# Performance work log

Hardware: AMD Instinct MI355X
Metric: run time of the kernel (lower is better)

## Reference

```python
import jax, jax.numpy as jnp
import numpy as np

N = 100000
E = 1600000
D = 64

def setup_inputs() -> dict:
    key = jax.random.key(0)
    k1, k2, k3, k4, k5, k6 = jax.random.split(key, 6)
    h = jax.random.normal(k1, (N, D), dtype=jnp.float32)
    w = jax.random.uniform(k2, (E, 1), dtype=jnp.float32)
    src = jax.random.randint(k3, (E,), 0, N, dtype=jnp.int32)
    dst = jax.random.randint(k4, (E,), 0, N, dtype=jnp.int32)
    W = jax.random.normal(k5, (D, 2 * D), dtype=jnp.float32) / np.sqrt(2 * D)
    b = jax.random.normal(k6, (D,), dtype=jnp.float32) * 0.01
    return {"h": h, "w": w, "src": src, "dst": dst, "W": W, "b": b}

def reference(h, w, src, dst, W, b):
    # messages: per-edge weight times gathered source features  [E, D]
    m = w * h[src]
    # scatter-sum into destination nodes  [N, D]
    agg = jax.ops.segment_sum(m, dst, num_segments=N)
    # concat self + aggregated, then linear: [N, 2D] @ [2D, D] + b
    return jnp.concatenate([h, agg], axis=1) @ W.T + b
```

## Files before the change

kernel.cpp:

```cpp
#include <hip/hip_runtime.h>

#define D 64
#define CAP 32
#define WQ_BITS 15
#define WQ_MAX 32767.0f
#define NSHARDS 8

typedef int   int4v   __attribute__((ext_vector_type(4)));
typedef float float4v __attribute__((ext_vector_type(4)));

__device__ __forceinline__ ushort f2bf(float x) {
    unsigned u = __float_as_uint(x);
    unsigned r = (u + 0x7fff + ((u >> 16) & 1)) >> 16;
    return (ushort)r;
}
__device__ __forceinline__ float bf2f(ushort u) {
    return __uint_as_float(((unsigned)u) << 16);
}

__global__ __launch_bounds__(256) void scatter_shard_kernel(
    const int* __restrict__ src, const int* __restrict__ dst,
    const float* __restrict__ w, int* __restrict__ cursor,
    unsigned* __restrict__ ovBits, unsigned* __restrict__ pairs,
    int E, int N)
{
    int shard   = blockIdx.x & (NSHARDS - 1);
    int slice   = blockIdx.x >> 3;
    int nSlices = gridDim.x >> 3;
    int n8 = (N + NSHARDS - 1) / NSHARDS;
    int lo = shard * n8;
    int hi = min(N, lo + n8);

    int e4 = E >> 2;
    for (int gi = slice * 256 + threadIdx.x; gi < e4; gi += nSlices * 256) {
        int e0 = gi * 4;
        int4v   d4 = __builtin_nontemporal_load((const int4v*)&dst[e0]);
        int4v   s4 = __builtin_nontemporal_load((const int4v*)&src[e0]);
        float4v w4 = __builtin_nontemporal_load((const float4v*)&w[e0]);
        #pragma unroll
        for (int i = 0; i < 4; ++i) {
            int d = d4[i];
            if (d >= lo && d < hi) {
                int e = e0 + i;
                int pos = atomicAdd(&cursor[d], 1);
                if (pos < CAP) {
                    float wv = fminf(fmaxf(w4[i], 0.f), 1.f);
                    unsigned wq = (unsigned)(wv * WQ_MAX + 0.5f);
                    pairs[(size_t)d * CAP + pos] =
                        ((unsigned)s4[i] << WQ_BITS) | wq;
                } else {
                    atomicOr(&ovBits[e >> 5], 1u << (e & 31));
                }
            }
        }
    }
    for (int e = e4 * 4 + slice * 256 + threadIdx.x; e < E; e += nSlices * 256) {
        int d = dst[e];
        if (d >= lo && d < hi) {
            int pos = atomicAdd(&cursor[d], 1);
            if (pos < CAP) {
                float wv = fminf(fmaxf(w[e], 0.f), 1.f);
                unsigned wq = (unsigned)(wv * WQ_MAX + 0.5f);
                pairs[(size_t)d * CAP + pos] =
                    ((unsigned)src[e] << WQ_BITS) | wq;
            } else {
                atomicOr(&ovBits[e >> 5], 1u << (e & 31));
            }
        }
    }
}

__global__ __launch_bounds__(256) void gemm_fused_kernel(
    const float* __restrict__ h, const float* __restrict__ W,
    const float* __restrict__ b, float* __restrict__ out,
    ushort* __restrict__ g, int N)
{
    __shared__ float Wt[128 * 64];
    __shared__ float Xt[64 * 64];
    int tid = threadIdx.x;

    for (int idx = tid; idx < 128 * 64; idx += 256) {
        int j = idx & 63;
        int k = idx >> 6;
        Wt[k * 64 + j] = W[j * 128 + k];
    }

    int n0blk = blockIdx.x * 64;
    {
        int n = tid & 63;
        int krow = tid >> 6;
        int nn = min(n0blk + n, N - 1);
        #pragma unroll
        for (int c = 0; c < 4; ++c) {
            int k0 = (krow + c * 4) * 4;
            float4 v = *(const float4*)&h[(size_t)nn * D + k0];
            Xt[(k0 + 0) * 64 + n] = v.x;
            Xt[(k0 + 1) * 64 + n] = v.y;
            Xt[(k0 + 2) * 64 + n] = v.z;
            Xt[(k0 + 3) * 64 + n] = v.w;
        }
    }
    __syncthreads();

    int j0 = (tid & 15) * 4;
    int nb = (tid >> 4) * 4;

    float4 bv = *(const float4*)&b[j0];
    float accS[4][4], accG[4][4];
    #pragma unroll
    for (int i = 0; i < 4; ++i) {
        accS[i][0] = bv.x; accS[i][1] = bv.y; accS[i][2] = bv.z; accS[i][3] = bv.w;
        accG[i][0] = 0.f;  accG[i][1] = 0.f;  accG[i][2] = 0.f;  accG[i][3] = 0.f;
    }

    #pragma unroll 4
    for (int k = 0; k < 64; ++k) {
        float4 xv = *(const float4*)&Xt[k * 64 + nb];
        float4 w1 = *(const float4*)&Wt[k * 64 + j0];
        float4 w2 = *(const float4*)&Wt[(k + 64) * 64 + j0];
        #pragma unroll
        for (int i = 0; i < 4; ++i) {
            float x = (&xv.x)[i];
            accS[i][0] += x * w1.x; accS[i][1] += x * w1.y;
            accS[i][2] += x * w1.z; accS[i][3] += x * w1.w;
            accG[i][0] += x * w2.x; accG[i][1] += x * w2.y;
            accG[i][2] += x * w2.z; accG[i][3] += x * w2.w;
        }
    }

    #pragma unroll
    for (int i = 0; i < 4; ++i) {
        int n = n0blk + nb + i;
        if (n < N) {
            *(float4*)&out[(size_t)n * D + j0] =
                make_float4(accS[i][0], accS[i][1], accS[i][2], accS[i][3]);
            ushort4 gv;
            gv.x = f2bf(accG[i][0]); gv.y = f2bf(accG[i][1]);
            gv.z = f2bf(accG[i][2]); gv.w = f2bf(accG[i][3]);
            *(ushort4*)&g[(size_t)n * D + j0] = gv;
        }
    }
}

__global__ __launch_bounds__(256) void final_agg_kernel(
    const ushort* __restrict__ g, const unsigned* __restrict__ pairs,
    const int* __restrict__ cursor, float* __restrict__ out, int N)
{
    int wave = threadIdx.x >> 6;
    int lane = threadIdx.x & 63;
    int n = blockIdx.x * 4 + wave;
    if (n >= N) return;
    int cnt = min(cursor[n], CAP);
    unsigned mycode = (lane < CAP) ? pairs[(size_t)n * CAP + lane] : 0u;
    float acc = out[(size_t)n * D + lane];

    const float wscale = 1.0f / WQ_MAX;
    int j = 0;
    for (; j + 16 <= cnt; j += 16) {
        unsigned c[16];
        float v[16];
        #pragma unroll
        for (int u = 0; u < 16; ++u) c[u] = __shfl(mycode, j + u);
        #pragma unroll
        for (int u = 0; u < 16; ++u)
            v[u] = bf2f(g[(size_t)(c[u] >> WQ_BITS) * D + lane]);
        #pragma unroll
        for (int u = 0; u < 16; ++u)
            acc += (float)(c[u] & 0x7fffu) * wscale * v[u];
    }
    for (; j + 8 <= cnt; j += 8) {
        unsigned c[8];
        float v[8];
        #pragma unroll
        for (int u = 0; u < 8; ++u) c[u] = __shfl(mycode, j + u);
        #pragma unroll
        for (int u = 0; u < 8; ++u)
            v[u] = bf2f(g[(size_t)(c[u] >> WQ_BITS) * D + lane]);
        #pragma unroll
        for (int u = 0; u < 8; ++u)
            acc += (float)(c[u] & 0x7fffu) * wscale * v[u];
    }
    for (; j + 4 <= cnt; j += 4) {
        unsigned c[4];
        float v[4];
        #pragma unroll
        for (int u = 0; u < 4; ++u) c[u] = __shfl(mycode, j + u);
        #pragma unroll
        for (int u = 0; u < 4; ++u)
            v[u] = bf2f(g[(size_t)(c[u] >> WQ_BITS) * D + lane]);
        #pragma unroll
        for (int u = 0; u < 4; ++u)
            acc += (float)(c[u] & 0x7fffu) * wscale * v[u];
    }
    for (; j < cnt; ++j) {
        unsigned c = __shfl(mycode, j);
        acc += (float)(c & 0x7fffu) * wscale *
               bf2f(g[(size_t)(c >> WQ_BITS) * D + lane]);
    }
    out[(size_t)n * D + lane] = acc;
}

__global__ __launch_bounds__(256) void overflow_kernel(
    const unsigned* __restrict__ ovBits, const int* __restrict__ src,
    const int* __restrict__ dst, const float* __restrict__ w,
    const ushort* __restrict__ g, float* __restrict__ out, int numWords)
{
    int idx = blockIdx.x * 256 + threadIdx.x;
    for (int wi = idx; wi < numWords; wi += gridDim.x * 256) {
        unsigned bits = ovBits[wi];
        while (bits) {
            int bit = __ffs(bits) - 1;
            bits &= bits - 1;
            int e = wi * 32 + bit;
            int s = src[e], d = dst[e];
            float wv = w[e];
            for (int f = 0; f < D; ++f)
                atomicAdd(&out[(size_t)d * D + f], wv * bf2f(g[(size_t)s * D + f]));
        }
    }
}

__global__ __launch_bounds__(256) void edge_scatter_kernel(
    const float* __restrict__ h, const float* __restrict__ w,
    const int* __restrict__ src, const int* __restrict__ dst,
    float* __restrict__ agg, int E)
{
    int e = blockIdx.x * 4 + (threadIdx.x >> 6);
    int lane = threadIdx.x & 63;
    if (e >= E) return;
    float val = w[e] * h[(size_t)src[e] * D + lane];
    atomicAdd(&agg[(size_t)dst[e] * D + lane], val);
}

__global__ __launch_bounds__(256) void out_linear_kernel(
    const float* __restrict__ h, const float* __restrict__ agg,
    const float* __restrict__ W, const float* __restrict__ b,
    float* __restrict__ out, int N)
{
    __shared__ float Wt[128 * 64];
    int lane = threadIdx.x & 63;
    int waveInBlock = threadIdx.x >> 6;
    int wavesPerBlock = blockDim.x >> 6;
    for (int idx = threadIdx.x; idx < 128 * 64; idx += blockDim.x) {
        int j = idx & 63;
        int k = idx >> 6;
        Wt[k * 64 + j] = W[j * 128 + k];
    }
    __syncthreads();
    float bj = b[lane];
    int wavesPerGrid = gridDim.x * wavesPerBlock;
    for (int n = blockIdx.x * wavesPerBlock + waveInBlock; n < N; n += wavesPerGrid) {
        float hreg = h[(size_t)n * D + lane];
        float areg = agg[(size_t)n * D + lane];
        float acc = bj;
        #pragma unroll
        for (int k = 0; k < 64; ++k) {
            float hk = __shfl(hreg, k, 64);
            float ak = __shfl(areg, k, 64);
            acc += hk * Wt[k * 64 + lane];
            acc += ak * Wt[(k + 64) * 64 + lane];
        }
        out[(size_t)n * D + lane] = acc;
    }
}

extern "C" void kernel_launch(void* const* d_in, const int* in_sizes, int n_in,
                              void* d_out, int out_size, void* d_ws, size_t ws_size,
                              hipStream_t stream) {
    const float* h   = (const float*)d_in[0];
    const float* w   = (const float*)d_in[1];
    const int*   src = (const int*)d_in[2];
    const int*   dst = (const int*)d_in[3];
    const float* W   = (const float*)d_in[4];
    const float* b   = (const float*)d_in[5];
    float* out = (float*)d_out;

    int N = in_sizes[0] / D;
    int E = in_sizes[1];
    int numWords = (E + 31) / 32;

    auto align256 = [](size_t x) { return (x + 255) & ~(size_t)255; };
    size_t cursorB = align256((size_t)N * 4);
    size_t ovB     = align256((size_t)numWords * 4);
    size_t pairsB  = align256((size_t)N * CAP * 4);
    size_t gB      = align256((size_t)N * D * 2);
    size_t need = cursorB + ovB + pairsB + gB;

    if (ws_size >= need && N <= (1 << 17)) {
        char* p = (char*)d_ws;
        int*      cursor = (int*)p;       p += cursorB;
        unsigned* ovBits = (unsigned*)p;  p += ovB;
        unsigned* pairs  = (unsigned*)p;  p += pairsB;
        ushort*   g      = (ushort*)p;

        hipMemsetAsync(cursor, 0, cursorB + ovB, stream);

        scatter_shard_kernel<<<4096, 256, 0, stream>>>(src, dst, w, cursor,
                                                       ovBits, pairs, E, N);
        gemm_fused_kernel<<<(N + 63) / 64, 256, 0, stream>>>(h, W, b, out, g, N);
        final_agg_kernel<<<(N + 3) / 4, 256, 0, stream>>>(g, pairs, cursor, out, N);
        overflow_kernel<<<64, 256, 0, stream>>>(ovBits, src, dst, w, g, out, numWords);
    } else {
        float* agg = out;
        hipMemsetAsync(agg, 0, (size_t)N * D * 4, stream);
        edge_scatter_kernel<<<(E + 3) / 4, 256, 0, stream>>>(h, w, src, dst, agg, E);
        out_linear_kernel<<<2048, 256, 0, stream>>>(h, agg, W, b, out, N);
    }
}
```

Baseline: 254.0 us.

## Use per-XCD private edge buckets instead of destination-sharded scatter

Replaces the destination-sharded scatter, which made every block scan all edges and filter by node range, with a single pass in which each XCD writes into its own cursor and bucket arrays, indexed by the hardware XCC id. The aim is to keep the atomics local to each XCD's L2 and to read the edge list only once. The aggregation kernel now gathers from eight 8-slot buckets per node using a ballot mask. The cost is eight times the cursor memory, a larger memset, and more edges spilling to the overflow path when one XCD's bucket for a node gets more than 8 entries.

```diff
diff --git a/kernel.cpp b/kernel.cpp
--- a/kernel.cpp
+++ b/kernel.cpp
@@ -1,10 +1,11 @@
 #include <hip/hip_runtime.h>
 
 #define D 64
-#define CAP 32
 #define WQ_BITS 15
 #define WQ_MAX 32767.0f
 #define NSHARDS 8
+#define CAP32 32
+#define CAPX 8
 
 typedef int   int4v   __attribute__((ext_vector_type(4)));
 typedef float float4v __attribute__((ext_vector_type(4)));
@@ -17,8 +18,60 @@
 __device__ __forceinline__ float bf2f(ushort u) {
     return __uint_as_float(((unsigned)u) << 16);
 }
-
-__global__ __launch_bounds__(256) void scatter_shard_kernel(
+__device__ __forceinline__ unsigned get_xcc_id() {
+    unsigned x;
+    asm volatile("s_getreg_b32 %0, hwreg(HW_REG_XCC_ID)" : "=s"(x));
+    return x & 7u;
+}
+
+__global__ __launch_bounds__(256) void scatter_xcd_kernel(
+    const int* __restrict__ src, const int* __restrict__ dst,
+    const float* __restrict__ w, int* __restrict__ cursor,
+    unsigned* __restrict__ ovBits, unsigned* __restrict__ pairs,
+    int E, int N)
+{
+    unsigned xcc = get_xcc_id();
+    int*      mycur   = cursor + (size_t)xcc * N;
+    unsigned* mypairs = pairs  + (size_t)xcc * N * CAPX;
+
+    int e4 = E >> 2;
+    for (int gi = blockIdx.x * 256 + threadIdx.x; gi < e4;
+         gi += gridDim.x * 256) {
+        int e0 = gi * 4;
+        int4v   d4 = __builtin_nontemporal_load((const int4v*)&dst[e0]);
+        int4v   s4 = __builtin_nontemporal_load((const int4v*)&src[e0]);
+        float4v w4 = __builtin_nontemporal_load((const float4v*)&w[e0]);
+        #pragma unroll
+        for (int i = 0; i < 4; ++i) {
+            int d = d4[i];
+            int pos = atomicAdd(&mycur[d], 1);
+            if (pos < CAPX) {
+                float wv = fminf(fmaxf(w4[i], 0.f), 1.f);
+                unsigned wq = (unsigned)(wv * WQ_MAX + 0.5f);
+                mypairs[(size_t)d * CAPX + pos] =
+                    ((unsigned)s4[i] << WQ_BITS) | wq;
+            } else {
+                int e = e0 + i;
+                atomicOr(&ovBits[e >> 5], 1u << (e & 31));
+            }
+        }
+    }
+    for (int e = e4 * 4 + blockIdx.x * 256 + threadIdx.x; e < E;
+         e += gridDim.x * 256) {
+        int d = dst[e];
+        int pos = atomicAdd(&mycur[d], 1);
+        if (pos < CAPX) {
+            float wv = fminf(fmaxf(w[e], 0.f), 1.f);
+            unsigned wq = (unsigned)(wv * WQ_MAX + 0.5f);
+            mypairs[(size_t)d * CAPX + pos] =
+                ((unsigned)src[e] << WQ_BITS) | wq;
+        } else {
+            atomicOr(&ovBits[e >> 5], 1u << (e & 31));
+        }
+    }
+}
+
+__global__ __launch_bounds__(256) void shard_scatter_kernel(
     const int* __restrict__ src, const int* __restrict__ dst,
     const float* __restrict__ w, int* __restrict__ cursor,
     unsigned* __restrict__ ovBits, unsigned* __restrict__ pairs,
@@ -43,10 +96,10 @@
             if (d >= lo && d < hi) {
                 int e = e0 + i;
                 int pos = atomicAdd(&cursor[d], 1);
-                if (pos < CAP) {
+                if (pos < CAP32) {
                     float wv = fminf(fmaxf(w4[i], 0.f), 1.f);
                     unsigned wq = (unsigned)(wv * WQ_MAX + 0.5f);
-                    pairs[(size_t)d * CAP + pos] =
+                    pairs[(size_t)d * CAP32 + pos] =
                         ((unsigned)s4[i] << WQ_BITS) | wq;
                 } else {
                     atomicOr(&ovBits[e >> 5], 1u << (e & 31));
@@ -58,10 +111,10 @@
         int d = dst[e];
         if (d >= lo && d < hi) {
             int pos = atomicAdd(&cursor[d], 1);
-            if (pos < CAP) {
+            if (pos < CAP32) {
                 float wv = fminf(fmaxf(w[e], 0.f), 1.f);
                 unsigned wq = (unsigned)(wv * WQ_MAX + 0.5f);
-                pairs[(size_t)d * CAP + pos] =
+                pairs[(size_t)d * CAP32 + pos] =
                     ((unsigned)src[e] << WQ_BITS) | wq;
             } else {
                 atomicOr(&ovBits[e >> 5], 1u << (e & 31));
@@ -142,7 +195,7 @@
     }
 }
 
-__global__ __launch_bounds__(256) void final_agg_kernel(
+__global__ __launch_bounds__(256) void final_agg_xcd_kernel(
     const ushort* __restrict__ g, const unsigned* __restrict__ pairs,
     const int* __restrict__ cursor, float* __restrict__ out, int N)
 {
@@ -150,8 +203,50 @@
     int lane = threadIdx.x & 63;
     int n = blockIdx.x * 4 + wave;
     if (n >= N) return;
-    int cnt = min(cursor[n], CAP);
-    unsigned mycode = (lane < CAP) ? pairs[(size_t)n * CAP + lane] : 0u;
+
+    int x    = lane >> 3;
+    int slot = lane & 7;
+    int cnt_x = min(cursor[(size_t)x * N + n], CAPX);
+    unsigned mycode = pairs[((size_t)x * N + n) * CAPX + slot];
+    bool valid = slot < cnt_x;
+    unsigned long long m = __ballot(valid);
+
+    float acc = out[(size_t)n * D + lane];
+    const float wscale = 1.0f / WQ_MAX;
+
+    while (m) {
+        unsigned c[16];
+        float v[16];
+        int k = 0;
+        #pragma unroll
+        for (int u = 0; u < 16; ++u) {
+            if (m) {
+                int l = (int)__ffsll(m) - 1;
+                m &= m - 1;
+                c[u] = __shfl(mycode, l);
+                k = u + 1;
+            }
+        }
+        #pragma unroll
+        for (int u = 0; u < 16; ++u)
+            if (u < k) v[u] = bf2f(g[(size_t)(c[u] >> WQ_BITS) * D + lane]);
+        #pragma unroll
+        for (int u = 0; u < 16; ++u)
+            if (u < k) acc += (float)(c[u] & 0x7fffu) * wscale * v[u];
+    }
+    out[(size_t)n * D + lane] = acc;
+}
+
+__global__ __launch_bounds__(256) void final_agg32_kernel(
+    const ushort* __restrict__ g, const unsigned* __restrict__ pairs,
+    const int* __restrict__ cursor, float* __restrict__ out, int N)
+{
+    int wave = threadIdx.x >> 6;
+    int lane = threadIdx.x & 63;
+    int n = blockIdx.x * 4 + wave;
+    if (n >= N) return;
+    int cnt = min(cursor[n], CAP32);
+    unsigned mycode = (lane < CAP32) ? pairs[(size_t)n * CAP32 + lane] : 0u;
     float acc = out[(size_t)n * D + lane];
 
     const float wscale = 1.0f / WQ_MAX;
@@ -166,18 +261,6 @@
             v[u] = bf2f(g[(size_t)(c[u] >> WQ_BITS) * D + lane]);
         #pragma unroll
         for (int u = 0; u < 16; ++u)
-            acc += (float)(c[u] & 0x7fffu) * wscale * v[u];
-    }
-    for (; j + 8 <= cnt; j += 8) {
-        unsigned c[8];
-        float v[8];
-        #pragma unroll
-        for (int u = 0; u < 8; ++u) c[u] = __shfl(mycode, j + u);
-        #pragma unroll
-        for (int u = 0; u < 8; ++u)
-            v[u] = bf2f(g[(size_t)(c[u] >> WQ_BITS) * D + lane]);
-        #pragma unroll
-        for (int u = 0; u < 8; ++u)
             acc += (float)(c[u] & 0x7fffu) * wscale * v[u];
     }
     for (; j + 4 <= cnt; j += 4) {
@@ -280,26 +363,50 @@
     int numWords = (E + 31) / 32;
 
     auto align256 = [](size_t x) { return (x + 255) & ~(size_t)255; };
-    size_t cursorB = align256((size_t)N * 4);
-    size_t ovB     = align256((size_t)numWords * 4);
-    size_t pairsB  = align256((size_t)N * CAP * 4);
-    size_t gB      = align256((size_t)N * D * 2);
-    size_t need = cursorB + ovB + pairsB + gB;
-
-    if (ws_size >= need && N <= (1 << 17)) {
+    size_t ovB = align256((size_t)numWords * 4);
+    size_t gB  = align256((size_t)N * D * 2);
+
+    size_t cursorB1 = align256((size_t)N * 8 * 4);
+    size_t pairsB1  = align256((size_t)N * 8 * CAPX * 4);
+    size_t need1 = cursorB1 + ovB + pairsB1 + gB;
+    size_t cursorB2 = align256((size_t)N * 4);
+    size_t pairsB2  = align256((size_t)N * CAP32 * 4);
+    size_t need2 = cursorB2 + ovB + pairsB2 + gB;
+
+    if (ws_size >= need1 && N <= (1 << 17)) {
         char* p = (char*)d_ws;
-        int*      cursor = (int*)p;       p += cursorB;
+        int*      cursor = (int*)p;       p += cursorB1;
         unsigned* ovBits = (unsigned*)p;  p += ovB;
-        unsigned* pairs  = (unsigned*)p;  p += pairsB;
+        unsigned* pairs  = (unsigned*)p;  p += pairsB1;
         ushort*   g      = (ushort*)p;
 
-        hipMemsetAsync(cursor, 0, cursorB + ovB, stream);
-
-        scatter_shard_kernel<<<4096, 256, 0, stream>>>(src, dst, w, cursor,
+        hipMemsetAsync(cursor, 0, cursorB1 + ovB, stream);
+
+        int e4 = E >> 2;
+        int scatterBlocks = min(2048, max(1, (e4 + 255) / 256));
+        scatter_xcd_kernel<<<scatterBlocks, 256, 0, stream>>>(
+            src, dst, w, cursor, ovBits, pairs, E, N);
+        gemm_fused_kernel<<<(N + 63) / 64, 256, 0, stream>>>(h, W, b, out, g, N);
+        final_agg_xcd_kernel<<<(N + 3) / 4, 256, 0, stream>>>(g, pairs, cursor,
+                                                              out, N);
+        overflow_kernel<<<64, 256, 0, stream>>>(ovBits, src, dst, w, g, out,
+                                                numWords);
+    } else if (ws_size >= need2 && N <= (1 << 17)) {
+        char* p = (char*)d_ws;
+        int*      cursor = (int*)p;       p += cursorB2;
+        unsigned* ovBits = (unsigned*)p;  p += ovB;
+        unsigned* pairs  = (unsigned*)p;  p += pairsB2;
+        ushort*   g      = (ushort*)p;
+
+        hipMemsetAsync(cursor, 0, cursorB2 + ovB, stream);
+
+        shard_scatter_kernel<<<4096, 256, 0, stream>>>(src, dst, w, cursor,
                                                        ovBits, pairs, E, N);
         gemm_fused_kernel<<<(N + 63) / 64, 256, 0, stream>>>(h, W, b, out, g, N);
-        final_agg_kernel<<<(N + 3) / 4, 256, 0, stream>>>(g, pairs, cursor, out, N);
-        overflow_kernel<<<64, 256, 0, stream>>>(ovBits, src, dst, w, g, out, numWords);
+        final_agg32_kernel<<<(N + 3) / 4, 256, 0, stream>>>(g, pairs, cursor,
+                                                            out, N);
+        overflow_kernel<<<64, 256, 0, stream>>>(ovBits, src, dst, w, g, out,
+                                                numWords);
     } else {
         float* agg = out;
         hipMemsetAsync(agg, 0, (size_t)N * D * 4, stream);
```

Result: slower. 348.3 us (+37.2%).

## Gather bf16 source features inside GEMM instead of gathering projected messages

Applied to the files above, without the earlier changes.

Instead of projecting every node through the second half of W and then gathering those projected rows, the code now converts h to bf16 once and gathers the raw bf16 source rows into a shared-memory tile inside the GEMM kernel. That tile then takes part in a single fused GEMM against both halves of W. The separate final aggregation pass and its read-modify-write of out are removed, at the cost of an extra conversion kernel and gather latency inside the GEMM blocks, which use more shared memory and may run at lower occupancy. The overflow path now projects each gathered row through W with wave shuffles and issues one atomic per lane.

```diff
diff --git a/kernel.cpp b/kernel.cpp
--- a/kernel.cpp
+++ b/kernel.cpp
@@ -1,13 +1,14 @@
 #include <hip/hip_runtime.h>
 
 #define D 64
-#define CAP 32
 #define WQ_BITS 15
 #define WQ_MAX 32767.0f
 #define NSHARDS 8
-
-typedef int   int4v   __attribute__((ext_vector_type(4)));
-typedef float float4v __attribute__((ext_vector_type(4)));
+#define CAP32 32
+
+typedef int    int4v    __attribute__((ext_vector_type(4)));
+typedef float  float4v  __attribute__((ext_vector_type(4)));
+typedef ushort ushort8v __attribute__((ext_vector_type(8)));
 
 __device__ __forceinline__ ushort f2bf(float x) {
     unsigned u = __float_as_uint(x);
@@ -18,7 +19,7 @@
     return __uint_as_float(((unsigned)u) << 16);
 }
 
-__global__ __launch_bounds__(256) void scatter_shard_kernel(
+__global__ __launch_bounds__(256) void shard_scatter_kernel(
     const int* __restrict__ src, const int* __restrict__ dst,
     const float* __restrict__ w, int* __restrict__ cursor,
     unsigned* __restrict__ ovBits, unsigned* __restrict__ pairs,
@@ -43,10 +44,10 @@
             if (d >= lo && d < hi) {
                 int e = e0 + i;
                 int pos = atomicAdd(&cursor[d], 1);
-                if (pos < CAP) {
+                if (pos < CAP32) {
                     float wv = fminf(fmaxf(w4[i], 0.f), 1.f);
                     unsigned wq = (unsigned)(wv * WQ_MAX + 0.5f);
-                    pairs[(size_t)d * CAP + pos] =
+                    pairs[(size_t)d * CAP32 + pos] =
                         ((unsigned)s4[i] << WQ_BITS) | wq;
                 } else {
                     atomicOr(&ovBits[e >> 5], 1u << (e & 31));
@@ -58,10 +59,10 @@
         int d = dst[e];
         if (d >= lo && d < hi) {
             int pos = atomicAdd(&cursor[d], 1);
-            if (pos < CAP) {
+            if (pos < CAP32) {
                 float wv = fminf(fmaxf(w[e], 0.f), 1.f);
                 unsigned wq = (unsigned)(wv * WQ_MAX + 0.5f);
-                pairs[(size_t)d * CAP + pos] =
+                pairs[(size_t)d * CAP32 + pos] =
                     ((unsigned)src[e] << WQ_BITS) | wq;
             } else {
                 atomicOr(&ovBits[e >> 5], 1u << (e & 31));
@@ -70,22 +71,39 @@
     }
 }
 
-__global__ __launch_bounds__(256) void gemm_fused_kernel(
+__global__ __launch_bounds__(256) void hbf_kernel(
+    const float* __restrict__ h, ushort* __restrict__ hbf, int total8)
+{
+    for (int i = blockIdx.x * 256 + threadIdx.x; i < total8;
+         i += gridDim.x * 256) {
+        float4 a = *(const float4*)&h[(size_t)i * 8];
+        float4 c = *(const float4*)&h[(size_t)i * 8 + 4];
+        ushort8v v;
+        v[0] = f2bf(a.x); v[1] = f2bf(a.y); v[2] = f2bf(a.z); v[3] = f2bf(a.w);
+        v[4] = f2bf(c.x); v[5] = f2bf(c.y); v[6] = f2bf(c.z); v[7] = f2bf(c.w);
+        *(ushort8v*)&hbf[(size_t)i * 8] = v;
+    }
+}
+
+__global__ __launch_bounds__(256) void gemm_gather_kernel(
     const float* __restrict__ h, const float* __restrict__ W,
-    const float* __restrict__ b, float* __restrict__ out,
-    ushort* __restrict__ g, int N)
+    const float* __restrict__ b, const ushort* __restrict__ hbf,
+    const unsigned* __restrict__ pairs, const int* __restrict__ cursor,
+    float* __restrict__ out, int N)
 {
     __shared__ float Wt[128 * 64];
     __shared__ float Xt[64 * 64];
-    int tid = threadIdx.x;
+    __shared__ float At[64 * 68];
+    int tid  = threadIdx.x;
+    int lane = tid & 63;
+    int wv   = tid >> 6;
+    int n0blk = blockIdx.x * 64;
 
     for (int idx = tid; idx < 128 * 64; idx += 256) {
         int j = idx & 63;
         int k = idx >> 6;
         Wt[k * 64 + j] = W[j * 128 + k];
     }
-
-    int n0blk = blockIdx.x * 64;
     {
         int n = tid & 63;
         int krow = tid >> 6;
@@ -100,31 +118,75 @@
             Xt[(k0 + 3) * 64 + n] = v.w;
         }
     }
+
+    const float wscale = 1.0f / WQ_MAX;
+    for (int ln = wv * 16; ln < wv * 16 + 16; ++ln) {
+        int n = n0blk + ln;
+        int cnt = 0;
+        unsigned mycode = 0;
+        if (n < N) {
+            cnt = min(cursor[n], CAP32);
+            if (lane < CAP32) mycode = pairs[(size_t)n * CAP32 + lane];
+        }
+        float acc = 0.f;
+        int j = 0;
+        for (; j + 16 <= cnt; j += 16) {
+            unsigned c[16];
+            float v[16];
+            #pragma unroll
+            for (int u = 0; u < 16; ++u) c[u] = __shfl(mycode, j + u);
+            #pragma unroll
+            for (int u = 0; u < 16; ++u)
+                v[u] = bf2f(hbf[(size_t)(c[u] >> WQ_BITS) * D + lane]);
+            #pragma unroll
+            for (int u = 0; u < 16; ++u)
+                acc += (float)(c[u] & 0x7fffu) * wscale * v[u];
+        }
+        for (; j + 4 <= cnt; j += 4) {
+            unsigned c[4];
+            float v[4];
+            #pragma unroll
+            for (int u = 0; u < 4; ++u) c[u] = __shfl(mycode, j + u);
+            #pragma unroll
+            for (int u = 0; u < 4; ++u)
+                v[u] = bf2f(hbf[(size_t)(c[u] >> WQ_BITS) * D + lane]);
+            #pragma unroll
+            for (int u = 0; u < 4; ++u)
+                acc += (float)(c[u] & 0x7fffu) * wscale * v[u];
+        }
+        for (; j < cnt; ++j) {
+            unsigned c = __shfl(mycode, j);
+            acc += (float)(c & 0x7fffu) * wscale *
+                   bf2f(hbf[(size_t)(c >> WQ_BITS) * D + lane]);
+        }
+        At[lane * 68 + ln] = acc;
+    }
     __syncthreads();
 
     int j0 = (tid & 15) * 4;
     int nb = (tid >> 4) * 4;
 
     float4 bv = *(const float4*)&b[j0];
-    float accS[4][4], accG[4][4];
+    float acc[4][4];
     #pragma unroll
     for (int i = 0; i < 4; ++i) {
-        accS[i][0] = bv.x; accS[i][1] = bv.y; accS[i][2] = bv.z; accS[i][3] = bv.w;
-        accG[i][0] = 0.f;  accG[i][1] = 0.f;  accG[i][2] = 0.f;  accG[i][3] = 0.f;
+        acc[i][0] = bv.x; acc[i][1] = bv.y; acc[i][2] = bv.z; acc[i][3] = bv.w;
     }
 
     #pragma unroll 4
     for (int k = 0; k < 64; ++k) {
         float4 xv = *(const float4*)&Xt[k * 64 + nb];
+        float4 av = *(const float4*)&At[k * 68 + nb];
         float4 w1 = *(const float4*)&Wt[k * 64 + j0];
         float4 w2 = *(const float4*)&Wt[(k + 64) * 64 + j0];
         #pragma unroll
         for (int i = 0; i < 4; ++i) {
             float x = (&xv.x)[i];
-            accS[i][0] += x * w1.x; accS[i][1] += x * w1.y;
-            accS[i][2] += x * w1.z; accS[i][3] += x * w1.w;
-            accG[i][0] += x * w2.x; accG[i][1] += x * w2.y;
-            accG[i][2] += x * w2.z; accG[i][3] += x * w2.w;
+            float a = (&av.x)[i];
+            acc[i][0] += x * w1.x + a * w2.x;
+            acc[i][1] += x * w1.y + a * w2.y;
+            acc[i][2] += x * w1.z + a * w2.z;
+            acc[i][3] += x * w1.w + a * w2.w;
         }
     }
 
@@ -133,89 +195,36 @@
         int n = n0blk + nb + i;
         if (n < N) {
             *(float4*)&out[(size_t)n * D + j0] =
-                make_float4(accS[i][0], accS[i][1], accS[i][2], accS[i][3]);
-            ushort4 gv;
-            gv.x = f2bf(accG[i][0]); gv.y = f2bf(accG[i][1]);
-            gv.z = f2bf(accG[i][2]); gv.w = f2bf(accG[i][3]);
-            *(ushort4*)&g[(size_t)n * D + j0] = gv;
-        }
-    }
-}
-
-__global__ __launch_bounds__(256) void final_agg_kernel(
-    const ushort* __restrict__ g, const unsigned* __restrict__ pairs,
-    const int* __restrict__ cursor, float* __restrict__ out, int N)
-{
-    int wave = threadIdx.x >> 6;
-    int lane = threadIdx.x & 63;
-    int n = blockIdx.x * 4 + wave;
-    if (n >= N) return;
-    int cnt = min(cursor[n], CAP);
-    unsigned mycode = (lane < CAP) ? pairs[(size_t)n * CAP + lane] : 0u;
-    float acc = out[(size_t)n * D + lane];
-
-    const float wscale = 1.0f / WQ_MAX;
-    int j = 0;
-    for (; j + 16 <= cnt; j += 16) {
-        unsigned c[16];
-        float v[16];
-        #pragma unroll
-        for (int u = 0; u < 16; ++u) c[u] = __shfl(mycode, j + u);
-        #pragma unroll
-        for (int u = 0; u < 16; ++u)
-            v[u] = bf2f(g[(size_t)(c[u] >> WQ_BITS) * D + lane]);
-        #pragma unroll
-        for (int u = 0; u < 16; ++u)
-            acc += (float)(c[u] & 0x7fffu) * wscale * v[u];
-    }
-    for (; j + 8 <= cnt; j += 8) {
-        unsigned c[8];
-        float v[8];
-        #pragma unroll
-        for (int u = 0; u < 8; ++u) c[u] = __shfl(mycode, j + u);
-        #pragma unroll
-        for (int u = 0; u < 8; ++u)
-            v[u] = bf2f(g[(size_t)(c[u] >> WQ_BITS) * D + lane]);
-        #pragma unroll
-        for (int u = 0; u < 8; ++u)
-            acc += (float)(c[u] & 0x7fffu) * wscale * v[u];
-    }
-    for (; j + 4 <= cnt; j += 4) {
-        unsigned c[4];
-        float v[4];
-        #pragma unroll
-        for (int u = 0; u < 4; ++u) c[u] = __shfl(mycode, j + u);
-        #pragma unroll
-        for (int u = 0; u < 4; ++u)
-            v[u] = bf2f(g[(size_t)(c[u] >> WQ_BITS) * D + lane]);
-        #pragma unroll
-        for (int u = 0; u < 4; ++u)
-            acc += (float)(c[u] & 0x7fffu) * wscale * v[u];
-    }
-    for (; j < cnt; ++j) {
-        unsigned c = __shfl(mycode, j);
-        acc += (float)(c & 0x7fffu) * wscale *
-               bf2f(g[(size_t)(c >> WQ_BITS) * D + lane]);
-    }
-    out[(size_t)n * D + lane] = acc;
-}
-
-__global__ __launch_bounds__(256) void overflow_kernel(
+                make_float4(acc[i][0], acc[i][1], acc[i][2], acc[i][3]);
+        }
+    }
+}
+
+__global__ __launch_bounds__(256) void overflow_fix_kernel(
     const unsigned* __restrict__ ovBits, const int* __restrict__ src,
     const int* __restrict__ dst, const float* __restrict__ w,
-    const ushort* __restrict__ g, float* __restrict__ out, int numWords)
-{
-    int idx = blockIdx.x * 256 + threadIdx.x;
-    for (int wi = idx; wi < numWords; wi += gridDim.x * 256) {
+    const ushort* __restrict__ hbf, const float* __restrict__ W,
+    float* __restrict__ out, int numWords)
+{
+    int lane   = threadIdx.x & 63;
+    int gwave  = (blockIdx.x * 256 + threadIdx.x) >> 6;
+    int nwaves = (gridDim.x * 256) >> 6;
+    for (int wi = gwave; wi < numWords; wi += nwaves) {
         unsigned bits = ovBits[wi];
         while (bits) {
             int bit = __ffs(bits) - 1;
             bits &= bits - 1;
             int e = wi * 32 + bit;
             int s = src[e], d = dst[e];
-            float wv = w[e];
-            for (int f = 0; f < D; ++f)
-                atomicAdd(&out[(size_t)d * D + f], wv * bf2f(g[(size_t)s * D + f]));
+            float wvv = w[e];
+            float hs = bf2f(hbf[(size_t)s * D + lane]);
+            float acc = 0.f;
+            #pragma unroll 8
+            for (int k = 0; k < 64; ++k) {
+                float hk = __shfl(hs, k, 64);
+                acc += hk * W[lane * 128 + 64 + k];
+            }
+            atomicAdd(&out[(size_t)d * D + lane], wvv * acc);
         }
     }
 }
@@ -282,24 +291,26 @@
     auto align256 = [](size_t x) { return (x + 255) & ~(size_t)255; };
     size_t cursorB = align256((size_t)N * 4);
     size_t ovB     = align256((size_t)numWords * 4);
-    size_t pairsB  = align256((size_t)N * CAP * 4);
-    size_t gB      = align256((size_t)N * D * 2);
-    size_t need = cursorB + ovB + pairsB + gB;
+    size_t pairsB  = align256((size_t)N * CAP32 * 4);
+    size_t hbfB    = align256((size_t)N * D * 2);
+    size_t need = cursorB + ovB + pairsB + hbfB;
 
     if (ws_size >= need && N <= (1 << 17)) {
         char* p = (char*)d_ws;
         int*      cursor = (int*)p;       p += cursorB;
         unsigned* ovBits = (unsigned*)p;  p += ovB;
         unsigned* pairs  = (unsigned*)p;  p += pairsB;
-        ushort*   g      = (ushort*)p;
+        ushort*   hbf    = (ushort*)p;
 
         hipMemsetAsync(cursor, 0, cursorB + ovB, stream);
 
-        scatter_shard_kernel<<<4096, 256, 0, stream>>>(src, dst, w, cursor,
+        hbf_kernel<<<2048, 256, 0, stream>>>(h, hbf, N * D / 8);
+        shard_scatter_kernel<<<4096, 256, 0, stream>>>(src, dst, w, cursor,
                                                        ovBits, pairs, E, N);
-        gemm_fused_kernel<<<(N + 63) / 64, 256, 0, stream>>>(h, W, b, out, g, N);
-        final_agg_kernel<<<(N + 3) / 4, 256, 0, stream>>>(g, pairs, cursor, out, N);
-        overflow_kernel<<<64, 256, 0, stream>>>(ovBits, src, dst, w, g, out, numWords);
+        gemm_gather_kernel<<<(N + 63) / 64, 256, 0, stream>>>(
+            h, W, b, hbf, pairs, cursor, out, N);
+        overflow_fix_kernel<<<64, 256, 0, stream>>>(ovBits, src, dst, w, hbf,
+                                                    W, out, numWords);
     } else {
         float* agg = out;
         hipMemsetAsync(agg, 0, (size_t)N * D * 4, stream);
```

New measurement: 388.1 us. +52.8%, slower.

## Merge scatter and GEMM kernels into one launch with block-range dispatch

Applied to the files above, without the earlier changes.

The edge scatter/bucketing kernel and the node GEMM kernel are independent, so they are merged into one launch: the first gemmB blocks run the GEMM and the remaining 4096 blocks run the sharded scatter. This removes a launch boundary and lets the compute-bound GEMM overlap with the atomic-heavy scatter. The scatter blocks now also reserve 48KB of shared memory they never use, which may lower their occupancy. The 8-wide unrolled tail loop in the aggregation kernel is also removed.

```diff
diff --git a/kernel.cpp b/kernel.cpp
--- a/kernel.cpp
+++ b/kernel.cpp
@@ -1,13 +1,14 @@
 #include <hip/hip_runtime.h>
 
 #define D 64
-#define CAP 32
 #define WQ_BITS 15
 #define WQ_MAX 32767.0f
 #define NSHARDS 8
-
-typedef int   int4v   __attribute__((ext_vector_type(4)));
-typedef float float4v __attribute__((ext_vector_type(4)));
+#define SCB 4096
+#define CAP32 32
+
+typedef int    int4v    __attribute__((ext_vector_type(4)));
+typedef float  float4v  __attribute__((ext_vector_type(4)));
 
 __device__ __forceinline__ ushort f2bf(float x) {
     unsigned u = __float_as_uint(x);
@@ -18,126 +19,127 @@
     return __uint_as_float(((unsigned)u) << 16);
 }
 
-__global__ __launch_bounds__(256) void scatter_shard_kernel(
+__global__ __launch_bounds__(256) void combined_kernel(
     const int* __restrict__ src, const int* __restrict__ dst,
     const float* __restrict__ w, int* __restrict__ cursor,
     unsigned* __restrict__ ovBits, unsigned* __restrict__ pairs,
-    int E, int N)
-{
-    int shard   = blockIdx.x & (NSHARDS - 1);
-    int slice   = blockIdx.x >> 3;
-    int nSlices = gridDim.x >> 3;
-    int n8 = (N + NSHARDS - 1) / NSHARDS;
-    int lo = shard * n8;
-    int hi = min(N, lo + n8);
-
-    int e4 = E >> 2;
-    for (int gi = slice * 256 + threadIdx.x; gi < e4; gi += nSlices * 256) {
-        int e0 = gi * 4;
-        int4v   d4 = __builtin_nontemporal_load((const int4v*)&dst[e0]);
-        int4v   s4 = __builtin_nontemporal_load((const int4v*)&src[e0]);
-        float4v w4 = __builtin_nontemporal_load((const float4v*)&w[e0]);
+    const float* __restrict__ h, const float* __restrict__ W,
+    const float* __restrict__ b, float* __restrict__ out,
+    ushort* __restrict__ g, int E, int N, int gemmB)
+{
+    __shared__ float Wt[128 * 64];
+    __shared__ float Xt[64 * 64];
+
+    if ((int)blockIdx.x < gemmB) {
+        int tid = threadIdx.x;
+        for (int idx = tid; idx < 128 * 64; idx += 256) {
+            int j = idx & 63;
+            int k = idx >> 6;
+            Wt[k * 64 + j] = W[j * 128 + k];
+        }
+        int n0blk = blockIdx.x * 64;
+        {
+            int n = tid & 63;
+            int krow = tid >> 6;
+            int nn = min(n0blk + n, N - 1);
+            #pragma unroll
+            for (int c = 0; c < 4; ++c) {
+                int k0 = (krow + c * 4) * 4;
+                float4 v = *(const float4*)&h[(size_t)nn * D + k0];
+                Xt[(k0 + 0) * 64 + n] = v.x;
+                Xt[(k0 + 1) * 64 + n] = v.y;
+                Xt[(k0 + 2) * 64 + n] = v.z;
+                Xt[(k0 + 3) * 64 + n] = v.w;
+            }
+        }
+        __syncthreads();
+
+        int j0 = (tid & 15) * 4;
+        int nb = (tid >> 4) * 4;
+
+        float4 bv = *(const float4*)&b[j0];
+        float accS[4][4], accG[4][4];
         #pragma unroll
         for (int i = 0; i < 4; ++i) {
-            int d = d4[i];
+            accS[i][0] = bv.x; accS[i][1] = bv.y;
+            accS[i][2] = bv.z; accS[i][3] = bv.w;
+            accG[i][0] = 0.f;  accG[i][1] = 0.f;
+            accG[i][2] = 0.f;  accG[i][3] = 0.f;
+        }
+
+        #pragma unroll 4
+        for (int k = 0; k < 64; ++k) {
+            float4 xv = *(const float4*)&Xt[k * 64 + nb];
+            float4 w1 = *(const float4*)&Wt[k * 64 + j0];
+            float4 w2 = *(const float4*)&Wt[(k + 64) * 64 + j0];
+            #pragma unroll
+            for (int i = 0; i < 4; ++i) {
+                float x = (&xv.x)[i];
+                accS[i][0] += x * w1.x; accS[i][1] += x * w1.y;
+                accS[i][2] += x * w1.z; accS[i][3] += x * w1.w;
+                accG[i][0] += x * w2.x; accG[i][1] += x * w2.y;
+                accG[i][2] += x * w2.z; accG[i][3] += x * w2.w;
+            }
+        }
+
+        #pragma unroll
+        for (int i = 0; i < 4; ++i) {
+            int n = n0blk + nb + i;
+            if (n < N) {
+                *(float4*)&out[(size_t)n * D + j0] =
+                    make_float4(accS[i][0], accS[i][1], accS[i][2], accS[i][3]);
+                ushort4 gv;
+                gv.x = f2bf(accG[i][0]); gv.y = f2bf(accG[i][1]);
+                gv.z = f2bf(accG[i][2]); gv.w = f2bf(accG[i][3]);
+                *(ushort4*)&g[(size_t)n * D + j0] = gv;
+            }
+        }
+    } else {
+        int bid     = blockIdx.x - gemmB;
+        int shard   = bid & (NSHARDS - 1);
+        int slice   = bid >> 3;
+        int nSlices = SCB >> 3;
+        int n8 = (N + NSHARDS - 1) / NSHARDS;
+        int lo = shard * n8;
+        int hi = min(N, lo + n8);
+
+        int e4 = E >> 2;
+        for (int gi = slice * 256 + threadIdx.x; gi < e4; gi += nSlices * 256) {
+            int e0 = gi * 4;
+            int4v   d4 = __builtin_nontemporal_load((const int4v*)&dst[e0]);
+            int4v   s4 = __builtin_nontemporal_load((const int4v*)&src[e0]);
+            float4v w4 = __builtin_nontemporal_load((const float4v*)&w[e0]);
+            #pragma unroll
+            for (int i = 0; i < 4; ++i) {
+                int d = d4[i];
+                if (d >= lo && d < hi) {
+                    int e = e0 + i;
+                    int pos = atomicAdd(&cursor[d], 1);
+                    if (pos < CAP32) {
+                        float wv = fminf(fmaxf(w4[i], 0.f), 1.f);
+                        unsigned wq = (unsigned)(wv * WQ_MAX + 0.5f);
+                        pairs[(size_t)d * CAP32 + pos] =
+                            ((unsigned)s4[i] << WQ_BITS) | wq;
+                    } else {
+                        atomicOr(&ovBits[e >> 5], 1u << (e & 31));
+                    }
+                }
+            }
+        }
+        for (int e = e4 * 4 + slice * 256 + threadIdx.x; e < E;
+             e += nSlices * 256) {
+            int d = dst[e];
             if (d >= lo && d < hi) {
-                int e = e0 + i;
                 int pos = atomicAdd(&cursor[d], 1);
-                if (pos < CAP) {
-                    float wv = fminf(fmaxf(w4[i], 0.f), 1.f);
+                if (pos < CAP32) {
+                    float wv = fminf(fmaxf(w[e], 0.f), 1.f);
                     unsigned wq = (unsigned)(wv * WQ_MAX + 0.5f);
-                    pairs[(size_t)d * CAP + pos] =
-                        ((unsigned)s4[i] << WQ_BITS) | wq;
+                    pairs[(size_t)d * CAP32 + pos] =
+                        ((unsigned)src[e] << WQ_BITS) | wq;
                 } else {
                     atomicOr(&ovBits[e >> 5], 1u << (e & 31));
                 }
             }
-        }
-    }
-    for (int e = e4 * 4 + slice * 256 + threadIdx.x; e < E; e += nSlices * 256) {
-        int d = dst[e];
-        if (d >= lo && d < hi) {
-            int pos = atomicAdd(&cursor[d], 1);
-            if (pos < CAP) {
-                float wv = fminf(fmaxf(w[e], 0.f), 1.f);
-                unsigned wq = (unsigned)(wv * WQ_MAX + 0.5f);
-                pairs[(size_t)d * CAP + pos] =
-                    ((unsigned)src[e] << WQ_BITS) | wq;
-            } else {
-                atomicOr(&ovBits[e >> 5], 1u << (e & 31));
-            }
-        }
-    }
-}
-
-__global__ __launch_bounds__(256) void gemm_fused_kernel(
-    const float* __restrict__ h, const float* __restrict__ W,
-    const float* __restrict__ b, float* __restrict__ out,
-    ushort* __restrict__ g, int N)
-{
-    __shared__ float Wt[128 * 64];
-    __shared__ float Xt[64 * 64];
-    int tid = threadIdx.x;
-
-    for (int idx = tid; idx < 128 * 64; idx += 256) {
-        int j = idx & 63;
-        int k = idx >> 6;
-        Wt[k * 64 + j] = W[j * 128 + k];
-    }
-
-    int n0blk = blockIdx.x * 64;
-    {
-        int n = tid & 63;
-        int krow = tid >> 6;
-        int nn = min(n0blk + n, N - 1);
-        #pragma unroll
-        for (int c = 0; c < 4; ++c) {
-            int k0 = (krow + c * 4) * 4;
-            float4 v = *(const float4*)&h[(size_t)nn * D + k0];
-            Xt[(k0 + 0) * 64 + n] = v.x;
-            Xt[(k0 + 1) * 64 + n] = v.y;
-            Xt[(k0 + 2) * 64 + n] = v.z;
-            Xt[(k0 + 3) * 64 + n] = v.w;
-        }
-    }
-    __syncthreads();
-
-    int j0 = (tid & 15) * 4;
-    int nb = (tid >> 4) * 4;
-
-    float4 bv = *(const float4*)&b[j0];
-    float accS[4][4], accG[4][4];
-    #pragma unroll
-    for (int i = 0; i < 4; ++i) {
-        accS[i][0] = bv.x; accS[i][1] = bv.y; accS[i][2] = bv.z; accS[i][3] = bv.w;
-        accG[i][0] = 0.f;  accG[i][1] = 0.f;  accG[i][2] = 0.f;  accG[i][3] = 0.f;
-    }
-
-    #pragma unroll 4
-    for (int k = 0; k < 64; ++k) {
-        float4 xv = *(const float4*)&Xt[k * 64 + nb];
-        float4 w1 = *(const float4*)&Wt[k * 64 + j0];
-        float4 w2 = *(const float4*)&Wt[(k + 64) * 64 + j0];
-        #pragma unroll
-        for (int i = 0; i < 4; ++i) {
-            float x = (&xv.x)[i];
-            accS[i][0] += x * w1.x; accS[i][1] += x * w1.y;
-            accS[i][2] += x * w1.z; accS[i][3] += x * w1.w;
-            accG[i][0] += x * w2.x; accG[i][1] += x * w2.y;
-            accG[i][2] += x * w2.z; accG[i][3] += x * w2.w;
-        }
-    }
-
-    #pragma unroll
-    for (int i = 0; i < 4; ++i) {
-        int n = n0blk + nb + i;
-        if (n < N) {
-            *(float4*)&out[(size_t)n * D + j0] =
-                make_float4(accS[i][0], accS[i][1], accS[i][2], accS[i][3]);
-            ushort4 gv;
-            gv.x = f2bf(accG[i][0]); gv.y = f2bf(accG[i][1]);
-            gv.z = f2bf(accG[i][2]); gv.w = f2bf(accG[i][3]);
-            *(ushort4*)&g[(size_t)n * D + j0] = gv;
         }
     }
 }
@@ -150,8 +152,8 @@
     int lane = threadIdx.x & 63;
     int n = blockIdx.x * 4 + wave;
     if (n >= N) return;
-    int cnt = min(cursor[n], CAP);
-    unsigned mycode = (lane < CAP) ? pairs[(size_t)n * CAP + lane] : 0u;
+    int cnt = min(cursor[n], CAP32);
+    unsigned mycode = (lane < CAP32) ? pairs[(size_t)n * CAP32 + lane] : 0u;
     float acc = out[(size_t)n * D + lane];
 
     const float wscale = 1.0f / WQ_MAX;
@@ -166,18 +168,6 @@
             v[u] = bf2f(g[(size_t)(c[u] >> WQ_BITS) * D + lane]);
         #pragma unroll
         for (int u = 0; u < 16; ++u)
-            acc += (float)(c[u] & 0x7fffu) * wscale * v[u];
-    }
-    for (; j + 8 <= cnt; j += 8) {
-        unsigned c[8];
-        float v[8];
-        #pragma unroll
-        for (int u = 0; u < 8; ++u) c[u] = __shfl(mycode, j + u);
-        #pragma unroll
-        for (int u = 0; u < 8; ++u)
-            v[u] = bf2f(g[(size_t)(c[u] >> WQ_BITS) * D + lane]);
-        #pragma unroll
-        for (int u = 0; u < 8; ++u)
             acc += (float)(c[u] & 0x7fffu) * wscale * v[u];
     }
     for (; j + 4 <= cnt; j += 4) {
@@ -282,7 +272,7 @@
     auto align256 = [](size_t x) { return (x + 255) & ~(size_t)255; };
     size_t cursorB = align256((size_t)N * 4);
     size_t ovB     = align256((size_t)numWords * 4);
-    size_t pairsB  = align256((size_t)N * CAP * 4);
+    size_t pairsB  = align256((size_t)N * CAP32 * 4);
     size_t gB      = align256((size_t)N * D * 2);
     size_t need = cursorB + ovB + pairsB + gB;
 
@@ -295,11 +285,13 @@
 
         hipMemsetAsync(cursor, 0, cursorB + ovB, stream);
 
-        scatter_shard_kernel<<<4096, 256, 0, stream>>>(src, dst, w, cursor,
-                                                       ovBits, pairs, E, N);
-        gemm_fused_kernel<<<(N + 63) / 64, 256, 0, stream>>>(h, W, b, out, g, N);
-        final_agg_kernel<<<(N + 3) / 4, 256, 0, stream>>>(g, pairs, cursor, out, N);
-        overflow_kernel<<<64, 256, 0, stream>>>(ovBits, src, dst, w, g, out, numWords);
+        int gemmB = (N + 63) / 64;
+        combined_kernel<<<gemmB + SCB, 256, 0, stream>>>(
+            src, dst, w, cursor, ovBits, pairs, h, W, b, out, g, E, N, gemmB);
+        final_agg_kernel<<<(N + 3) / 4, 256, 0, stream>>>(g, pairs, cursor,
+                                                          out, N);
+        overflow_kernel<<<64, 256, 0, stream>>>(ovBits, src, dst, w, g, out,
+                                                numWords);
     } else {
         float* agg = out;
         hipMemsetAsync(agg, 0, (size_t)N * D * 4, stream);
```

Result: slower. 261.5 us (+3.0%).
